# Optimization experiments

Hardware: AMD Instinct MI355X
Metric: run time of the kernel (lower is better)

The kernel has to match this reference:

```python
import jax, jax.numpy as jnp
from jax import lax
import numpy as np

N, C, H, W = 8, 128, 96, 96
G, K = 8, 3                      # groups, kernel_size
GC = C // G                      # group channels = 16
STRIDE, PAD, DIL = 1, 1, 1
OFFSET_SCALE = 1.0
OM_DIM = int(np.ceil(G * K * K * 3 / 8) * 8)   # 216 (== G*K*K*3, no padding)
GN_EPS = 1e-5


def setup_inputs() -> dict:
    key = jax.random.key(0)
    ks = jax.random.split(key, 7)
    inp = {
        "input": jax.random.normal(ks[0], (N, C, H, W), dtype=jnp.float32),
        # depthwise conv (Conv2d groups=C): OIHW with I=1
        "dw_w": jax.random.normal(ks[1], (C, 1, K, K), dtype=jnp.float32) * 0.1,
        "dw_b": jax.random.normal(ks[2], (C,), dtype=jnp.float32) * 0.05,
        # GroupNorm(num_groups=1) affine params
        "gn_w": jnp.ones((C,), dtype=jnp.float32),
        "gn_b": jnp.zeros((C,), dtype=jnp.float32),
        # offset_mask Linear (module zero-inits; use small random for a meaningful test)
        "om_w": jax.random.normal(ks[3], (OM_DIM, C), dtype=jnp.float32) * 0.02,
        "om_b": jax.random.normal(ks[4], (OM_DIM,), dtype=jnp.float32) * 0.02,
    }
    return inp


def _dcnv4_forward(x, dw_w, dw_b, gn_w, gn_b, om_w, om_b):
    # x: (N, C, H, W)
    # ---- offset/mask branch: depthwise conv -> GroupNorm(1) -> GELU -> Linear
    x1 = lax.conv_general_dilated(
        x, dw_w, window_strides=(1, 1), padding=[(1, 1), (1, 1)],
        feature_group_count=C, dimension_numbers=("NCHW", "OIHW", "NCHW"))
    x1 = x1 + dw_b[None, :, None, None]
    mu = jnp.mean(x1, axis=(1, 2, 3), keepdims=True)
    var = jnp.var(x1, axis=(1, 2, 3), keepdims=True)
    x1 = (x1 - mu) * lax.rsqrt(var + GN_EPS)
    x1 = x1 * gn_w[None, :, None, None] + gn_b[None, :, None, None]
    x1 = jax.nn.gelu(x1, approximate=False)
    x1 = jnp.transpose(x1, (0, 2, 3, 1))                     # (N,H,W,C)
    om = jnp.einsum("nhwc,oc->nhwo", x1, om_w) + om_b        # (N,H,W,216)

    K2 = K * K
    om = om[..., : G * K2 * 3].reshape(N, H, W, G, K2 * 3)
    offs = om[..., : 2 * K2].reshape(N, H, W, G, K2, 2)      # (dx, dy) per point
    mask = om[..., 2 * K2:]                                  # (N,H,W,G,K2), no softmax in DCNv4

    # ---- sampling locations (pixel coords in the unpadded input, zeros outside)
    ky, kx = jnp.meshgrid(jnp.arange(K), jnp.arange(K), indexing="ij")
    base_y = ((ky - (K - 1) / 2.0) * DIL).reshape(-1).astype(jnp.float32)  # (K2,)
    base_x = ((kx - (K - 1) / 2.0) * DIL).reshape(-1).astype(jnp.float32)
    ctr_y = jnp.arange(H, dtype=jnp.float32) * STRIDE - PAD + DIL * (K - 1) / 2.0
    ctr_x = jnp.arange(W, dtype=jnp.float32) * STRIDE - PAD + DIL * (K - 1) / 2.0
    loc_y = ctr_y[None, :, None, None, None] + (base_y + offs[..., 1]) * OFFSET_SCALE
    loc_x = ctr_x[None, None, :, None, None] + (base_x + offs[..., 0]) * OFFSET_SCALE

    # ---- grouped bilinear gather
    xv = jnp.transpose(x, (0, 2, 3, 1)).reshape(N, H, W, G, GC)   # values, channels-last
    y0 = jnp.floor(loc_y)
    x0 = jnp.floor(loc_x)
    ly = loc_y - y0
    lx = loc_x - x0
    y0i = y0.astype(jnp.int32)
    x0i = x0.astype(jnp.int32)
    n_idx = jnp.arange(N)[:, None, None, None, None]
    g_idx = jnp.arange(G)[None, None, None, :, None]

    def gather(yi, xi):
        valid = (yi >= 0) & (yi < H) & (xi >= 0) & (xi < W)
        yc = jnp.clip(yi, 0, H - 1)
        xc = jnp.clip(xi, 0, W - 1)
        v = xv[n_idx, yc, xc, g_idx]                 # (N,H,W,G,K2,GC)
        return v * valid[..., None].astype(xv.dtype)

    samp = (gather(y0i,     x0i)     * ((1 - ly) * (1 - lx))[..., None]
          + gather(y0i,     x0i + 1) * ((1 - ly) * lx)[..., None]
          + gather(y0i + 1, x0i)     * (ly * (1 - lx))[..., None]
          + gather(y0i + 1, x0i + 1) * (ly * lx)[..., None])

    out = jnp.sum(samp * mask[..., None], axis=4)    # (N,H,W,G,GC)
    out = out.reshape(N, H, W, C)
    return jnp.transpose(out, (0, 3, 1, 2))          # (N,C,H,W)


def reference(input, dw_w, dw_b, gn_w, gn_b, om_w, om_b):
    return _dcnv4_forward(input, dw_w, dw_b, gn_w, gn_b, om_w, om_b)
```

## Files before the change

### kernel.cpp

```cpp
#include <hip/hip_runtime.h>
#include <hip/hip_bf16.h>

#define N_   8
#define C_   128
#define H_   96
#define W_   96
#define G_   8
#define GC_  16
#define HW_  (H_ * W_)
#define CHW_ (C_ * HW_)
#define OM_  216
#define OMP_ 224
#define OMROWS2_ 112
#define EPS_ 1e-5f
#define BLKS_PER_N_ 192
#define PW_  100
#define PPLANE_ (PW_ * PW_ * GC_)

typedef short bf16x8 __attribute__((ext_vector_type(8)));
typedef float f32x4 __attribute__((ext_vector_type(4)));

#if __has_builtin(__builtin_amdgcn_fdot2_f32_bf16)
#define HAVE_DOT2_ 1
typedef __bf16 bf16x2 __attribute__((ext_vector_type(2)));
static __device__ __forceinline__ bf16x2 u2bf2(unsigned int u) {
  union { unsigned int i; bf16x2 v; } c;
  c.i = u;
  return c.v;
}
#else
#define HAVE_DOT2_ 0
#endif

static __device__ __forceinline__ unsigned short f2bf(float f) {
  unsigned int u = __float_as_uint(f);
  unsigned int r = (u + 0x7fffu + ((u >> 16) & 1u)) >> 16;
  return (unsigned short)r;
}
static __device__ __forceinline__ unsigned int pk_bf2(float lo, float hi) {
  __hip_bfloat162 h = __float22bfloat162_rn(make_float2(lo, hi));
  union { __hip_bfloat162 h; unsigned int u; } c;
  c.h = h;
  return c.u;
}
static __device__ __forceinline__ float lo_bf(unsigned int u) {
  return __uint_as_float(u << 16);
}
static __device__ __forceinline__ float hi_bf(unsigned int u) {
  return __uint_as_float(u & 0xffff0000u);
}

static __device__ __forceinline__ float fast_gelu(float z) {
  float s = z * 0.70710678118654752f;
  float as = fabsf(s);
  float t = __builtin_amdgcn_rcpf(fmaf(0.3275911f, as, 1.0f));
  float e = __expf(-as * as);
  float inner = fmaf(fmaf(fmaf(fmaf(1.061405429f, t, -1.453152027f), t,
                               1.421413741f), t, -0.284496736f), t, 0.254829592f);
  float y = fmaf(-inner * t, e, 1.0f);
  float erf_s = copysignf(y, s);
  float hz = 0.5f * z;
  return fmaf(hz, erf_s, hz);
}

static __device__ __forceinline__ void loadrow5(float dst[2][5],
                                                const float* __restrict__ xp0,
                                                const float* __restrict__ xp1,
                                                int hh, int w0) {
  bool vy = (hh >= 0) & (hh < H_);
#pragma unroll
  for (int j = 0; j < 5; ++j) {
    int ww = w0 - 1 + j;
    bool v = vy & (ww >= 0) & (ww < W_);
    dst[0][j] = v ? xp0[hh * W_ + ww] : 0.0f;
    dst[1][j] = v ? xp1[hh * W_ + ww] : 0.0f;
  }
}

__global__ __launch_bounds__(256) void k_front(const float* __restrict__ x,
                                               const float* __restrict__ dw_w,
                                               const float* __restrict__ dw_b,
                                               unsigned short* __restrict__ xgb,
                                               unsigned short* __restrict__ x1b,
                                               float2* __restrict__ partials,
                                               const float* __restrict__ om_w,
                                               const float* __restrict__ om_b,
                                               unsigned short* __restrict__ A,
                                               float* __restrict__ biasp) {
  int fb = blockIdx.x;
  int tid = threadIdx.x;

  if (fb >= N_ * BLKS_PER_N_) {
    int pb2 = fb - N_ * BLKS_PER_N_;
    if (pb2 < 112) {
      int idx = pb2 * 256 + tid;
      int o = idx >> 7;
      int cix = idx & 127;
      int g = o / 28;
      int k = o - g * 28;
      float v = (k < 27) ? om_w[(g * 27 + k) * C_ + cix] : 0.0f;
      A[idx] = f2bf(v);
      if (cix == 0) biasp[o] = (k < 27) ? om_b[g * 27 + k] : 0.0f;
    } else {
      int gid = (pb2 - 112) * 256 + tid;
      const int NBORD = 64 * 784;
      for (int id = gid; id < NBORD; id += 80 * 256) {
        int plane = id / 784;
        int r = id - plane * 784;
        int row, col;
        if (r < 400) {
          int qq = r / 100;
          row = (qq < 2) ? qq : qq + 96;
          col = r - qq * 100;
        } else {
          int r2 = r - 400;
          int qq = r2 >> 2;
          int c4 = r2 & 3;
          row = 2 + qq;
          col = (c4 < 2) ? c4 : c4 + 96;
        }
        uint4* dst = (uint4*)(xgb + (size_t)plane * PPLANE_ + (row * PW_ + col) * GC_);
        uint4 z = {0, 0, 0, 0};
        dst[0] = z;
        dst[1] = z;
      }
    }
    return;
  }

  __shared__ unsigned int lds_c[384 * 9];
  __shared__ unsigned int lds_a[384 * 9];
  __shared__ float ls[4], lq[4];

  int tx = tid & 31;
  int ty = tid >> 5;
  int n   = fb / BLKS_PER_N_;
  int rem = fb - n * BLKS_PER_N_;
  int g   = rem / 24;
  int hb  = rem - g * 24;
  int h0 = hb * 4;
  int w0 = tx * 3;

  const int c0 = g * 16 + 2 * ty;
  float wk[2][9];
  const float* wp = dw_w + c0 * 9;
#pragma unroll
  for (int j = 0; j < 9; ++j) {
    wk[0][j] = wp[j];
    wk[1][j] = wp[9 + j];
  }
  float bias[2] = {dw_b[c0], dw_b[c0 + 1]};

  const float* xp0 = x + ((size_t)(n * C_ + c0)) * HW_;
  const float* xp1 = xp0 + HW_;

  float s = 0.0f, q = 0.0f;

  float rr[3][2][5];
  loadrow5(rr[0], xp0, xp1, h0 - 1, w0);
  loadrow5(rr[1], xp0, xp1, h0,     w0);

#pragma unroll
  for (int r = 0; r < 4; ++r) {
    const int sA = r % 3;
    const int sB = (r + 1) % 3;
    const int sC = (r + 2) % 3;
    loadrow5(rr[sC], xp0, xp1, h0 + r + 1, w0);

#pragma unroll
    for (int j = 0; j < 3; ++j) {
      float acc0 = bias[0], acc1 = bias[1];
#pragma unroll
      for (int dx = 0; dx < 3; ++dx) {
        acc0 = fmaf(rr[sA][0][j + dx], wk[0][0 + dx], acc0);
        acc1 = fmaf(rr[sA][1][j + dx], wk[1][0 + dx], acc1);
        acc0 = fmaf(rr[sB][0][j + dx], wk[0][3 + dx], acc0);
        acc1 = fmaf(rr[sB][1][j + dx], wk[1][3 + dx], acc1);
        acc0 = fmaf(rr[sC][0][j + dx], wk[0][6 + dx], acc0);
        acc1 = fmaf(rr[sC][1][j + dx], wk[1][6 + dx], acc1);
      }
      float cen0 = rr[sB][0][j + 1];
      float cen1 = rr[sB][1][j + 1];
      s += acc0 + acc1;
      q = fmaf(acc0, acc0, q);
      q = fmaf(acc1, acc1, q);
      int pxl = r * 96 + w0 + j;
      lds_a[pxl * 9 + ty] = pk_bf2(acc0, acc1);
      lds_c[pxl * 9 + ty] = pk_bf2(cen0, cen1);
    }
  }
  __syncthreads();

  for (int i = tid; i < 384; i += 256) {
    int row = i / 96;
    int col = i - row * 96;
    unsigned int wc[8], wa[8];
#pragma unroll
    for (int k = 0; k < 8; ++k) {
      wc[k] = lds_c[i * 9 + k];
      wa[k] = lds_a[i * 9 + k];
    }
    unsigned int* xg = (unsigned int*)xgb + (size_t)(n * G_ + g) * (PPLANE_ / 2)
                       + ((h0 + row + 2) * PW_ + (col + 2)) * 8;
    uint4 c01 = {wc[0], wc[1], wc[2], wc[3]};
    uint4 c23 = {wc[4], wc[5], wc[6], wc[7]};
    *(uint4*)xg = c01;
    *(uint4*)(xg + 4) = c23;
    int p = (h0 + row) * W_ + col;
    unsigned int* xb = (unsigned int*)x1b + ((size_t)n * HW_ + p) * 64 + g * 8;
    uint4 a01 = {wa[0], wa[1], wa[2], wa[3]};
    uint4 a23 = {wa[4], wa[5], wa[6], wa[7]};
    *(uint4*)xb = a01;
    *(uint4*)(xb + 4) = a23;
  }

#pragma unroll
  for (int o = 32; o > 0; o >>= 1) {
    s += __shfl_down(s, o);
    q += __shfl_down(q, o);
  }
  int lane = tid & 63;
  int wv = tid >> 6;
  if (lane == 0) { ls[wv] = s; lq[wv] = q; }
  __syncthreads();
  if (tid == 0) {
    partials[fb] = make_float2(ls[0] + ls[1] + ls[2] + ls[3],
                               lq[0] + lq[1] + lq[2] + lq[3]);
  }
}

static __device__ __forceinline__ void pref_af(bf16x8 (&af)[4],
                                               const unsigned short* __restrict__ A,
                                               int ot, int l16, int quad) {
  const unsigned short* Ap = A + (ot * 16 + l16) * C_ + quad * 8;
#pragma unroll
  for (int kk = 0; kk < 4; ++kk) af[kk] = *(const bf16x8*)(Ap + kk * 32);
}

__global__ __launch_bounds__(256) void k_gemm_mfma(const unsigned short* __restrict__ Bt,
                                                   const unsigned short* __restrict__ A,
                                                   const float* __restrict__ biasp,
                                                   const float2* __restrict__ partials,
                                                   const float* __restrict__ gn_w,
                                                   const float* __restrict__ gn_b,
                                                   unsigned int* __restrict__ om2) {
  __shared__ unsigned short Bl[32 * 136];
  __shared__ alignas(16) float s_bias[OMP_];
  __shared__ float ls[4], lq[4];
  int tid = threadIdx.x;
  int pb = blockIdx.x;
  int n = blockIdx.y;
  int p0 = pb * 32;

  const unsigned short* src = Bt + ((size_t)n * HW_ + p0) * C_;
  int col = tid & 15;
  int row0 = tid >> 4;
  uint4 raw0 = *(const uint4*)(src + row0 * C_ + col * 8);
  uint4 raw1 = *(const uint4*)(src + (16 + row0) * C_ + col * 8);
  int cbase = col * 8;
  float gw8[8], gb8[8];
#pragma unroll
  for (int j = 0; j < 8; ++j) {
    gw8[j] = gn_w[cbase + j];
    gb8[j] = gn_b[cbase + j];
  }
  if (tid < OMP_ / 4) {
    ((float4*)s_bias)[tid] = ((const float4*)biasp)[tid];
  }

  {
    float s = 0.0f, q = 0.0f;
    if (tid < BLKS_PER_N_) {
      float2 v = partials[n * BLKS_PER_N_ + tid];
      s = v.x;
      q = v.y;
    }
#pragma unroll
    for (int o = 32; o > 0; o >>= 1) {
      s += __shfl_down(s, o);
      q += __shfl_down(q, o);
    }
    int lane = tid & 63;
    int wv = tid >> 6;
    if (lane == 0) { ls[wv] = s; lq[wv] = q; }
  }
  __syncthreads();

  float sum = ls[0] + ls[1] + ls[2] + ls[3];
  float ssq = lq[0] + lq[1] + lq[2] + lq[3];
  const float inv = 1.0f / (float)CHW_;
  float mean = sum * inv;
  float var = ssq * inv - mean * mean;
  float rstd = rsqrtf(var + EPS_);
  float a8[8], b8[8];
#pragma unroll
  for (int j = 0; j < 8; ++j) {
    a8[j] = rstd * gw8[j];
    b8[j] = gb8[j] - mean * rstd * gw8[j];
  }

  {
    uint4 raws[2] = {raw0, raw1};
#pragma unroll
    for (int i = 0; i < 2; ++i) {
      int row = row0 + i * 16;
      unsigned int d[4] = {raws[i].x, raws[i].y, raws[i].z, raws[i].w};
      unsigned int od[4];
#pragma unroll
      for (int t = 0; t < 4; ++t) {
        float v0 = lo_bf(d[t]);
        float v1 = hi_bf(d[t]);
        float z0 = fmaf(v0, a8[2 * t], b8[2 * t]);
        float z1 = fmaf(v1, a8[2 * t + 1], b8[2 * t + 1]);
        od[t] = pk_bf2(fast_gelu(z0), fast_gelu(z1));
      }
      uint4 packed = {od[0], od[1], od[2], od[3]};
      *(uint4*)(&Bl[row * 136 + col * 8]) = packed;
    }
  }
  __syncthreads();

  int wave = tid >> 6;
  int lane = tid & 63;
  int quad = lane >> 4;
  int l16 = lane & 15;
  int pixhalf = wave & 1;
  int othalf = wave >> 1;
  int prow = pixhalf * 16 + l16;

  bf16x8 bfrag[4];
#pragma unroll
  for (int kk = 0; kk < 4; ++kk)
    bfrag[kk] = *(const bf16x8*)(&Bl[prow * 136 + kk * 32 + quad * 8]);

  int p = p0 + prow;
  int base = othalf * 7;

#define COMP_(AF, OT)                                                          \
  {                                                                            \
    f32x4 acc = {0.f, 0.f, 0.f, 0.f};                                          \
    _Pragma("unroll")                                                          \
    for (int kk = 0; kk < 4; ++kk)                                             \
      acc = __builtin_amdgcn_mfma_f32_16x16x32_bf16(AF[kk], bfrag[kk], acc,    \
                                                    0, 0, 0);                  \
    int o0 = (OT) * 16 + quad * 4;                                             \
    float4 bv = *(const float4*)(&s_bias[o0]);                                 \
    unsigned int pk0 = pk_bf2(acc[0] + bv.x, acc[1] + bv.y);                   \
    unsigned int pk1 = pk_bf2(acc[2] + bv.z, acc[3] + bv.w);                   \
    unsigned int* Cp = om2 + ((size_t)n * OMROWS2_ + (o0 >> 1)) * HW_ + p;     \
    Cp[0] = pk0;                                                               \
    Cp[HW_] = pk1;                                                             \
  }

  bf16x8 af0[4], af1[4];
  pref_af(af0, A, base + 0, l16, quad);
  pref_af(af1, A, base + 1, l16, quad);
  COMP_(af0, base + 0);
  pref_af(af0, A, base + 2, l16, quad);
  COMP_(af1, base + 1);
  pref_af(af1, A, base + 3, l16, quad);
  COMP_(af0, base + 2);
  pref_af(af0, A, base + 4, l16, quad);
  COMP_(af1, base + 3);
  pref_af(af1, A, base + 5, l16, quad);
  COMP_(af0, base + 4);
  pref_af(af0, A, base + 6, l16, quad);
  COMP_(af1, base + 5);
  COMP_(af0, base + 6);
#undef COMP_
}

__global__ __launch_bounds__(256, 4) void k_sample(const unsigned short* __restrict__ xgb,
                                                   const unsigned int* __restrict__ om2,
                                                   float* __restrict__ out) {
  __shared__ int4 s_wa[9 * 64];

  int tid = threadIdx.x;
  int ord = blockIdx.x;
  int n = ord & 7;
  int t2 = ord >> 3;
  int g = t2 & 7;
  int pb = t2 >> 3;
  int p0 = pb * 64;

  const unsigned int* omb = om2 + ((size_t)n * OMROWS2_ + g * 14) * HW_ + p0;
  for (int j = tid; j < 576; j += 256) {
    int pt = j >> 6;
    int px = j & 63;
    int p = p0 + px;
    int h = p / W_;
    int w = p - h * W_;
    unsigned int od = omb[pt * HW_ + px];
    float offx = lo_bf(od);
    float offy = hi_bf(od);
    unsigned int md = omb[(9 + (pt >> 1)) * HW_ + px];
    float m = (pt & 1) ? hi_bf(md) : lo_bf(md);
    float locy = (float)(h + pt / 3 - 1) + offy;
    float locx = (float)(w + pt % 3 - 1) + offx;
    float y0f = floorf(locy);
    float x0f = floorf(locx);
    float ly = locy - y0f;
    float lx = locx - x0f;
    int y0 = (int)y0f;
    int x0 = (int)x0f;
    y0 = min(max(y0, -2), 96);
    x0 = min(max(x0, -2), 96);
    float t0 = (1.0f - ly) * m;
    float t1 = ly * m;
    float u0 = 1.0f - lx;
    int4 wa;
    wa.x = (int)pk_bf2(t0 * u0, t1 * u0);
    wa.y = (int)pk_bf2(t0 * lx, t1 * lx);
    wa.z = ((y0 + 2) * PW_ + (x0 + 2)) * GC_;
    wa.w = wa.z + PW_ * GC_;
    s_wa[j] = wa;
  }
  __syncthreads();

  int px_l = tid >> 2;
  int sub = tid & 3;
  int rowhalf = sub >> 1;
  int chunk = sub & 1;
  int p = p0 + px_l;
  const unsigned short* xbb = xgb + (size_t)(n * G_ + g) * PPLANE_;

  float acc[8] = {0, 0, 0, 0, 0, 0, 0, 0};

  int4 wa = s_wa[px_l];
  uint4 r0 = *(const uint4*)(xbb + wa.z + sub * 8);
  uint4 r1 = *(const uint4*)(xbb + wa.w + sub * 8);

#pragma unroll
  for (int pt = 0; pt < 9; ++pt) {
    int4 wa_n;
    uint4 r0n, r1n;
    if (pt < 8) {
      wa_n = s_wa[(pt + 1) * 64 + px_l];
      r0n = *(const uint4*)(xbb + wa_n.z + sub * 8);
      r1n = *(const uint4*)(xbb + wa_n.w + sub * 8);
    }

    unsigned int aw = (unsigned int)(rowhalf ? wa.y : wa.x);
    unsigned int d0[4] = {r0.x, r0.y, r0.z, r0.w};
    unsigned int d1[4] = {r1.x, r1.y, r1.z, r1.w};
#if HAVE_DOT2_
    bf16x2 a2 = u2bf2(aw);
#pragma unroll
    for (int t = 0; t < 4; ++t) {
      unsigned int blo = __builtin_amdgcn_perm(d1[t], d0[t], 0x05040100u);
      unsigned int bhi = __builtin_amdgcn_perm(d1[t], d0[t], 0x07060302u);
      acc[2 * t]     = __builtin_amdgcn_fdot2_f32_bf16(a2, u2bf2(blo), acc[2 * t], false);
      acc[2 * t + 1] = __builtin_amdgcn_fdot2_f32_bf16(a2, u2bf2(bhi), acc[2 * t + 1], false);
    }
#else
    float w0 = lo_bf(aw);
    float w1 = hi_bf(aw);
#pragma unroll
    for (int t = 0; t < 4; ++t) {
      acc[2 * t]     = fmaf(w0, lo_bf(d0[t]), acc[2 * t]);
      acc[2 * t + 1] = fmaf(w0, hi_bf(d0[t]), acc[2 * t + 1]);
      acc[2 * t]     = fmaf(w1, lo_bf(d1[t]), acc[2 * t]);
      acc[2 * t + 1] = fmaf(w1, hi_bf(d1[t]), acc[2 * t + 1]);
    }
#endif
    if (pt < 8) {
      wa = wa_n;
      r0 = r0n;
      r1 = r1n;
    }
  }

#pragma unroll
  for (int i = 0; i < 8; ++i) acc[i] += __shfl_xor(acc[i], 2);

  int ch = chunk * 8 + rowhalf * 4;
  float* op = out + ((size_t)(n * C_ + g * GC_ + ch)) * HW_ + p;
#pragma unroll
  for (int r = 0; r < 4; ++r) op[r * HW_] = acc[rowhalf * 4 + r];
}

extern "C" void kernel_launch(void* const* d_in, const int* in_sizes, int n_in,
                              void* d_out, int out_size, void* d_ws, size_t ws_size,
                              hipStream_t stream) {
  const float* x    = (const float*)d_in[0];
  const float* dw_w = (const float*)d_in[1];
  const float* dw_b = (const float*)d_in[2];
  const float* gn_w = (const float*)d_in[3];
  const float* gn_b = (const float*)d_in[4];
  const float* om_w = (const float*)d_in[5];
  const float* om_b = (const float*)d_in[6];
  float* out = (float*)d_out;

  unsigned short* xgb = (unsigned short*)d_ws;
  unsigned short* x1b = xgb + (size_t)64 * PPLANE_;
  unsigned int* om2 = (unsigned int*)(x1b + (size_t)N_ * CHW_);
  float* stats = (float*)(om2 + (size_t)N_ * OMROWS2_ * HW_);
  float2* partials = (float2*)(stats + 16);
  unsigned short* Abf = (unsigned short*)(partials + N_ * BLKS_PER_N_);
  float* biasp = (float*)(Abf + OMP_ * C_);

  k_front<<<N_ * BLKS_PER_N_ + 192, 256, 0, stream>>>(
      x, dw_w, dw_b, xgb, x1b, partials, om_w, om_b, Abf, biasp);
  k_gemm_mfma<<<dim3(HW_ / 32, N_), 256, 0, stream>>>(
      x1b, Abf, biasp, partials, gn_w, gn_b, om2);
  k_sample<<<9216, 256, 0, stream>>>(xgb, om2, out);
}
```

Before: 183.6 us.

## Fuse offset/mask GEMM with deformable sampling via LDS handoff

Merges the MFMA offset/mask GEMM and the bilinear sampling kernel into one kernel. The GEMM writes its bf16 offset/mask tile into shared memory, and the same block then samples 32 pixels across all 8 groups. This removes the om2 global round trip and one launch. Each thread now computes all 16 channels of one pixel/group, replacing the 4-thread split and shuffle reduction. The cost is fewer threads for the gather phase (2304 blocks × 256 threads, one pixel-group each), no software prefetch, higher register pressure and more LDS per block, which may hurt latency hiding on the gather loads.

```diff
diff --git a/kernel.cpp b/kernel.cpp
--- a/kernel.cpp
+++ b/kernel.cpp
@@ -237,16 +237,18 @@
   for (int kk = 0; kk < 4; ++kk) af[kk] = *(const bf16x8*)(Ap + kk * 32);
 }
 
-__global__ __launch_bounds__(256) void k_gemm_mfma(const unsigned short* __restrict__ Bt,
-                                                   const unsigned short* __restrict__ A,
-                                                   const float* __restrict__ biasp,
-                                                   const float2* __restrict__ partials,
-                                                   const float* __restrict__ gn_w,
-                                                   const float* __restrict__ gn_b,
-                                                   unsigned int* __restrict__ om2) {
+__global__ __launch_bounds__(256) void k_gemm_sample(const unsigned short* __restrict__ Bt,
+                                                     const unsigned short* __restrict__ A,
+                                                     const float* __restrict__ biasp,
+                                                     const float2* __restrict__ partials,
+                                                     const float* __restrict__ gn_w,
+                                                     const float* __restrict__ gn_b,
+                                                     const unsigned short* __restrict__ xgb,
+                                                     float* __restrict__ out) {
   __shared__ unsigned short Bl[32 * 136];
   __shared__ alignas(16) float s_bias[OMP_];
   __shared__ float ls[4], lq[4];
+  __shared__ unsigned int om_lds[112 * 33];
   int tid = threadIdx.x;
   int pb = blockIdx.x;
   int n = blockIdx.y;
@@ -333,7 +335,6 @@
   for (int kk = 0; kk < 4; ++kk)
     bfrag[kk] = *(const bf16x8*)(&Bl[prow * 136 + kk * 32 + quad * 8]);
 
-  int p = p0 + prow;
   int base = othalf * 7;
 
 #define COMP_(AF, OT)                                                          \
@@ -347,9 +348,9 @@
     float4 bv = *(const float4*)(&s_bias[o0]);                                 \
     unsigned int pk0 = pk_bf2(acc[0] + bv.x, acc[1] + bv.y);                   \
     unsigned int pk1 = pk_bf2(acc[2] + bv.z, acc[3] + bv.w);                   \
-    unsigned int* Cp = om2 + ((size_t)n * OMROWS2_ + (o0 >> 1)) * HW_ + p;     \
-    Cp[0] = pk0;                                                               \
-    Cp[HW_] = pk1;                                                             \
+    int r2 = o0 >> 1;                                                          \
+    om_lds[r2 * 33 + prow] = pk0;                                              \
+    om_lds[(r2 + 1) * 33 + prow] = pk1;                                        \
   }
 
   bf16x8 af0[4], af1[4];
@@ -368,35 +369,32 @@
   COMP_(af1, base + 5);
   COMP_(af0, base + 6);
 #undef COMP_
-}
-
-__global__ __launch_bounds__(256, 4) void k_sample(const unsigned short* __restrict__ xgb,
-                                                   const unsigned int* __restrict__ om2,
-                                                   float* __restrict__ out) {
-  __shared__ int4 s_wa[9 * 64];
-
-  int tid = threadIdx.x;
-  int ord = blockIdx.x;
-  int n = ord & 7;
-  int t2 = ord >> 3;
-  int g = t2 & 7;
-  int pb = t2 >> 3;
-  int p0 = pb * 64;
-
-  const unsigned int* omb = om2 + ((size_t)n * OMROWS2_ + g * 14) * HW_ + p0;
-  for (int j = tid; j < 576; j += 256) {
-    int pt = j >> 6;
-    int px = j & 63;
-    int p = p0 + px;
-    int h = p / W_;
-    int w = p - h * W_;
-    unsigned int od = omb[pt * HW_ + px];
+
+  __syncthreads();
+
+  int spx = tid & 31;
+  int sg = tid >> 5;
+  int hb0 = p0 / W_;
+  int wb0 = p0 - hb0 * W_;
+  int wsum = wb0 + spx;
+  int carry = wsum >= W_;
+  int sh = hb0 + carry;
+  int sw = wsum - (carry ? W_ : 0);
+  const char* xs = (const char*)(xgb + (size_t)(n * G_ + sg) * PPLANE_);
+
+  float acc[16];
+#pragma unroll
+  for (int i = 0; i < 16; ++i) acc[i] = 0.f;
+
+#pragma unroll
+  for (int pt = 0; pt < 9; ++pt) {
+    unsigned int od = om_lds[(sg * 14 + pt) * 33 + spx];
+    unsigned int md = om_lds[(sg * 14 + 9 + (pt >> 1)) * 33 + spx];
     float offx = lo_bf(od);
     float offy = hi_bf(od);
-    unsigned int md = omb[(9 + (pt >> 1)) * HW_ + px];
     float m = (pt & 1) ? hi_bf(md) : lo_bf(md);
-    float locy = (float)(h + pt / 3 - 1) + offy;
-    float locx = (float)(w + pt % 3 - 1) + offx;
+    float locy = (float)(sh + pt / 3 - 1) + offy;
+    float locx = (float)(sw + pt % 3 - 1) + offx;
     float y0f = floorf(locy);
     float x0f = floorf(locx);
     float ly = locy - y0f;
@@ -408,75 +406,66 @@
     float t0 = (1.0f - ly) * m;
     float t1 = ly * m;
     float u0 = 1.0f - lx;
-    int4 wa;
-    wa.x = (int)pk_bf2(t0 * u0, t1 * u0);
-    wa.y = (int)pk_bf2(t0 * lx, t1 * lx);
-    wa.z = ((y0 + 2) * PW_ + (x0 + 2)) * GC_;
-    wa.w = wa.z + PW_ * GC_;
-    s_wa[j] = wa;
-  }
-  __syncthreads();
-
-  int px_l = tid >> 2;
-  int sub = tid & 3;
-  int rowhalf = sub >> 1;
-  int chunk = sub & 1;
-  int p = p0 + px_l;
-  const unsigned short* xbb = xgb + (size_t)(n * G_ + g) * PPLANE_;
-
-  float acc[8] = {0, 0, 0, 0, 0, 0, 0, 0};
-
-  int4 wa = s_wa[px_l];
-  uint4 r0 = *(const uint4*)(xbb + wa.z + sub * 8);
-  uint4 r1 = *(const uint4*)(xbb + wa.w + sub * 8);
-
-#pragma unroll
-  for (int pt = 0; pt < 9; ++pt) {
-    int4 wa_n;
-    uint4 r0n, r1n;
-    if (pt < 8) {
-      wa_n = s_wa[(pt + 1) * 64 + px_l];
-      r0n = *(const uint4*)(xbb + wa_n.z + sub * 8);
-      r1n = *(const uint4*)(xbb + wa_n.w + sub * 8);
-    }
-
-    unsigned int aw = (unsigned int)(rowhalf ? wa.y : wa.x);
-    unsigned int d0[4] = {r0.x, r0.y, r0.z, r0.w};
-    unsigned int d1[4] = {r1.x, r1.y, r1.z, r1.w};
+    int z0 = ((y0 + 2) * PW_ + (x0 + 2)) * (GC_ * 2);
+    int z1 = z0 + PW_ * GC_ * 2;
+    uint4 r0a = *(const uint4*)(xs + z0);
+    uint4 r0b = *(const uint4*)(xs + z0 + 16);
+    uint4 r0c = *(const uint4*)(xs + z0 + 32);
+    uint4 r0d = *(const uint4*)(xs + z0 + 48);
+    uint4 r1a = *(const uint4*)(xs + z1);
+    uint4 r1b = *(const uint4*)(xs + z1 + 16);
+    uint4 r1c = *(const uint4*)(xs + z1 + 32);
+    uint4 r1d = *(const uint4*)(xs + z1 + 48);
 #if HAVE_DOT2_
-    bf16x2 a2 = u2bf2(aw);
-#pragma unroll
-    for (int t = 0; t < 4; ++t) {
-      unsigned int blo = __builtin_amdgcn_perm(d1[t], d0[t], 0x05040100u);
-      unsigned int bhi = __builtin_amdgcn_perm(d1[t], d0[t], 0x07060302u);
-      acc[2 * t]     = __builtin_amdgcn_fdot2_f32_bf16(a2, u2bf2(blo), acc[2 * t], false);
-      acc[2 * t + 1] = __builtin_amdgcn_fdot2_f32_bf16(a2, u2bf2(bhi), acc[2 * t + 1], false);
-    }
+    bf16x2 ac0 = u2bf2(pk_bf2(t0 * u0, t1 * u0));
+    bf16x2 ac1 = u2bf2(pk_bf2(t0 * lx, t1 * lx));
+#define ACC8_(A2, R0, R1, BASE)                                                \
+    {                                                                          \
+      unsigned int d0[4] = {(R0).x, (R0).y, (R0).z, (R0).w};                   \
+      unsigned int d1[4] = {(R1).x, (R1).y, (R1).z, (R1).w};                   \
+      _Pragma("unroll")                                                        \
+      for (int t = 0; t < 4; ++t) {                                            \
+        unsigned int blo = __builtin_amdgcn_perm(d1[t], d0[t], 0x05040100u);   \
+        unsigned int bhi = __builtin_amdgcn_perm(d1[t], d0[t], 0x07060302u);   \
+        acc[(BASE) + 2 * t]     = __builtin_amdgcn_fdot2_f32_bf16(             \
+            A2, u2bf2(blo), acc[(BASE) + 2 * t], false);                       \
+        acc[(BASE) + 2 * t + 1] = __builtin_amdgcn_fdot2_f32_bf16(             \
+            A2, u2bf2(bhi), acc[(BASE) + 2 * t + 1], false);                   \
+      }                                                                        \
+    }
+    ACC8_(ac0, r0a, r1a, 0);
+    ACC8_(ac0, r0b, r1b, 8);
+    ACC8_(ac1, r0c, r1c, 0);
+    ACC8_(ac1, r0d, r1d, 8);
+#undef ACC8_
 #else
-    float w0 = lo_bf(aw);
-    float w1 = hi_bf(aw);
-#pragma unroll
-    for (int t = 0; t < 4; ++t) {
-      acc[2 * t]     = fmaf(w0, lo_bf(d0[t]), acc[2 * t]);
-      acc[2 * t + 1] = fmaf(w0, hi_bf(d0[t]), acc[2 * t + 1]);
-      acc[2 * t]     = fmaf(w1, lo_bf(d1[t]), acc[2 * t]);
-      acc[2 * t + 1] = fmaf(w1, hi_bf(d1[t]), acc[2 * t + 1]);
-    }
+    unsigned int wc0 = pk_bf2(t0 * u0, t1 * u0);
+    unsigned int wc1 = pk_bf2(t0 * lx, t1 * lx);
+    float w00 = lo_bf(wc0), w10 = hi_bf(wc0);
+    float w01 = lo_bf(wc1), w11 = hi_bf(wc1);
+#define ACC8F_(W0, W1, R0, R1, BASE)                                           \
+    {                                                                          \
+      unsigned int d0[4] = {(R0).x, (R0).y, (R0).z, (R0).w};                   \
+      unsigned int d1[4] = {(R1).x, (R1).y, (R1).z, (R1).w};                   \
+      _Pragma("unroll")                                                        \
+      for (int t = 0; t < 4; ++t) {                                            \
+        acc[(BASE) + 2 * t]     = fmaf(W0, lo_bf(d0[t]), acc[(BASE) + 2 * t]); \
+        acc[(BASE) + 2 * t + 1] = fmaf(W0, hi_bf(d0[t]), acc[(BASE) + 2 * t + 1]); \
+        acc[(BASE) + 2 * t]     = fmaf(W1, lo_bf(d1[t]), acc[(BASE) + 2 * t]); \
+        acc[(BASE) + 2 * t + 1] = fmaf(W1, hi_bf(d1[t]), acc[(BASE) + 2 * t + 1]); \
+      }                                                                        \
+    }
+    ACC8F_(w00, w10, r0a, r1a, 0);
+    ACC8F_(w00, w10, r0b, r1b, 8);
+    ACC8F_(w01, w11, r0c, r1c, 0);
+    ACC8F_(w01, w11, r0d, r1d, 8);
+#undef ACC8F_
 #endif
-    if (pt < 8) {
-      wa = wa_n;
-      r0 = r0n;
-      r1 = r1n;
-    }
-  }
-
-#pragma unroll
-  for (int i = 0; i < 8; ++i) acc[i] += __shfl_xor(acc[i], 2);
-
-  int ch = chunk * 8 + rowhalf * 4;
-  float* op = out + ((size_t)(n * C_ + g * GC_ + ch)) * HW_ + p;
-#pragma unroll
-  for (int r = 0; r < 4; ++r) op[r * HW_] = acc[rowhalf * 4 + r];
+  }
+
+  float* op = out + ((size_t)(n * C_ + sg * GC_)) * HW_ + p0 + spx;
+#pragma unroll
+  for (int c = 0; c < 16; ++c) op[c * HW_] = acc[c];
 }
 
 extern "C" void kernel_launch(void* const* d_in, const int* in_sizes, int n_in,
@@ -493,15 +482,12 @@
 
   unsigned short* xgb = (unsigned short*)d_ws;
   unsigned short* x1b = xgb + (size_t)64 * PPLANE_;
-  unsigned int* om2 = (unsigned int*)(x1b + (size_t)N_ * CHW_);
-  float* stats = (float*)(om2 + (size_t)N_ * OMROWS2_ * HW_);
-  float2* partials = (float2*)(stats + 16);
+  float2* partials = (float2*)(x1b + (size_t)N_ * CHW_);
   unsigned short* Abf = (unsigned short*)(partials + N_ * BLKS_PER_N_);
   float* biasp = (float*)(Abf + OMP_ * C_);
 
   k_front<<<N_ * BLKS_PER_N_ + 192, 256, 0, stream>>>(
       x, dw_w, dw_b, xgb, x1b, partials, om_w, om_b, Abf, biasp);
-  k_gemm_mfma<<<dim3(HW_ / 32, N_), 256, 0, stream>>>(
-      x1b, Abf, biasp, partials, gn_w, gn_b, om2);
-  k_sample<<<9216, 256, 0, stream>>>(xgb, om2, out);
-}
+  k_gemm_sample<<<dim3(HW_ / 32, N_), 256, 0, stream>>>(
+      x1b, Abf, biasp, partials, gn_w, gn_b, xgb, out);
+}
```

Result: no change. 185.3 us (+0.9%).
